# Kernel tuning notes

Hardware: AMD Instinct MI355X
Metric: run time of the kernel (lower is better)

## Reference

```python
import jax, jax.numpy as jnp
import numpy as np

B, S, P, D, L = 8, 224, 14, 512, 6
NPS = S // P            # 16 patches per side
N = NPS * NPS           # 256 tokens
G = L - 1               # 5 feedforward groups
H = D * 4
TOKEN_ATTEND_SELF_VALUE = -0.0005


def setup_inputs() -> dict:
    key = jax.random.key(0)
    k = jax.random.split(key, 8)
    s = 0.02
    f = jnp.float32
    return {
        "img": jax.random.normal(k[0], (B, 3, S, S), f),
        "W_patch": jax.random.normal(k[1], (P * P * 3, D), f) * s,
        "b_patch": jnp.zeros((D,), f),
        "pos_emb": jax.random.normal(k[2], (N, D), f) * s,
        "init_levels": jax.random.normal(k[3], (L, D), f),
        "bu_W1": jax.random.normal(k[4], (G, D, H), f) * s,
        "bu_b1": jnp.zeros((G, H), f),
        "bu_W2": jax.random.normal(k[5], (G, H, D), f) * s,
        "bu_b2": jnp.zeros((G, D), f),
        "td_W1": jax.random.normal(k[6], (G, D, H), f) * s,
        "td_b1": jnp.zeros((G, H), f),
        "td_W2": jax.random.normal(k[7], (G, H, D), f) * s,
        "td_b2": jnp.zeros((G, D), f),
        "iters": 12,
    }


def _grouped_ff(x, W1, b1, W2, b2):
    # x: [b, n, G, d]; grouped 1x1 conv == independent per-level MLP
    h = jax.nn.gelu(jnp.einsum('bnld,ldh->bnlh', x, W1) + b1, approximate=False)
    return jnp.einsum('bnlh,lhd->bnld', h, W2) + b2


def _consensus(levels):
    # levels: [b, n, L, d]; q = levels, k = l2-normalized levels, v = levels
    d = levels.shape[-1]
    norm = jnp.maximum(jnp.linalg.norm(levels, axis=-1, keepdims=True), 1e-12)
    k = levels / norm
    sim = jnp.einsum('bild,bjld->blij', levels, k) * (d ** -0.5)
    n = levels.shape[1]
    eye = jnp.eye(n, dtype=bool)[None, None]
    sim = jnp.where(eye, TOKEN_ATTEND_SELF_VALUE, sim)  # attend_self=False
    attn = jax.nn.softmax(sim, axis=-1)
    return jnp.einsum('blij,bjld->bild', attn, levels)


def _forward(img, W_patch, b_patch, pos_emb, init_levels,
             bu_W1, bu_b1, bu_W2, bu_b2, td_W1, td_b1, td_W2, td_b2, iters):
    b = img.shape[0]
    # 'b c (h p1) (w p2) -> b (h w) (p1 p2 c)'
    x = img.reshape(b, 3, NPS, P, NPS, P).transpose(0, 2, 4, 3, 5, 1).reshape(b, N, P * P * 3)
    tokens = x @ W_patch + b_patch                  # [b, n, d]
    bottom = tokens[:, :, None, :]                  # [b, n, 1, d]
    levels = jnp.broadcast_to(init_levels, (b, N, L, D)).astype(img.dtype)
    pos = pos_emb[None, :, None, :]
    contrib = jnp.array([4.0] * (L - 1) + [3.0], jnp.float32).reshape(1, 1, L, 1)

    def step(lv, _):
        lw = jnp.concatenate([bottom, lv], axis=-2)                 # [b, n, L+1, d]
        bu = _grouped_ff(lw[..., 1:-1, :], bu_W1, bu_b1, bu_W2, bu_b2)
        td = _grouped_ff(lw[..., 2:, :] + pos, td_W1, td_b1, td_W2, td_b2)
        bu = jnp.concatenate([bottom, bu], axis=-2)                 # [b, n, L, d]
        td = jnp.pad(td, ((0, 0), (0, 0), (0, 1), (0, 0)))          # [b, n, L, d]
        cons = _consensus(lv)
        new = (lv + bu + td + cons) / contrib
        return new, None

    levels, _ = jax.lax.scan(step, levels, None, length=iters)
    return levels


def reference(img, W_patch, b_patch, pos_emb, init_levels,
              bu_W1, bu_b1, bu_W2, bu_b2, td_W1, td_b1, td_W2, td_b2, iters):
    return _forward(img, W_patch, b_patch, pos_emb, init_levels,
                    bu_W1, bu_b1, bu_W2, bu_b2, td_W1, td_b1, td_W2, td_b2, iters)
```

## Files before the change

kernel.cpp:

```cpp
#include <hip/hip_runtime.h>
#include <math.h>

#define L6 6

typedef __attribute__((ext_vector_type(8))) short bf16x8;
typedef __attribute__((ext_vector_type(4))) float f32x4;

#define SH_W_GRP   2097152ull
#define SH_A_GRP   2097152ull
#define SH_A_TDOFF 10485760ull

__device__ __forceinline__ float gelu_exact(float x) {
  return 0.5f * x * (1.0f + erff(x * 0.70710678118654752f));
}

__device__ __forceinline__ unsigned short bf16_rn(float x) {
  unsigned u = __float_as_uint(x);
  unsigned r = u + 0x7FFFu + ((u >> 16) & 1u);
  return (unsigned short)(r >> 16);
}
__device__ __forceinline__ float bf16_f(unsigned short h) {
  return __uint_as_float(((unsigned)h) << 16);
}
__device__ __forceinline__ void split2(float x, unsigned short* h, unsigned short* l) {
  unsigned short hh = bf16_rn(x);
  *h = hh;
  *l = bf16_rn(x - bf16_f(hh));
}
__device__ __forceinline__ int4 pack8(const unsigned short* v) {
  return make_int4((int)((unsigned)v[0] | ((unsigned)v[1] << 16)),
                   (int)((unsigned)v[2] | ((unsigned)v[3] << 16)),
                   (int)((unsigned)v[4] | ((unsigned)v[5] << 16)),
                   (int)((unsigned)v[6] | ((unsigned)v[7] << 16)));
}

__device__ __forceinline__ void gload16(const void* g, void* l) {
  __builtin_amdgcn_global_load_lds(
      (const __attribute__((address_space(1))) void*)g,
      (__attribute__((address_space(3))) void*)l, 16, 0, 0);
}

__global__ __launch_bounds__(256) void patch_embed(
    const float* __restrict__ img, const float* __restrict__ Wp,
    const float* __restrict__ bp, float* __restrict__ tokens)
{
  __shared__ float xs[588];
  const int bn = blockIdx.x;
  const int b = bn >> 8, n = bn & 255;
  const int i = n >> 4, j = n & 15;
  for (int k = threadIdx.x; k < 588; k += 256) {
    int c = k % 3;
    int t = k / 3;
    int pc = t % 14;
    int pr = t / 14;
    xs[k] = img[(((size_t)(b * 3 + c) * 224) + (i * 14 + pr)) * 224 + (j * 14 + pc)];
  }
  __syncthreads();
  const int d0 = threadIdx.x, d1 = threadIdx.x + 256;
  float a0 = 0.f, a1 = 0.f;
  for (int k = 0; k < 588; ++k) {
    float x = xs[k];
    a0 = fmaf(x, Wp[(size_t)k * 512 + d0], a0);
    a1 = fmaf(x, Wp[(size_t)k * 512 + d1], a1);
  }
  tokens[(size_t)bn * 512 + d0] = a0 + bp[d0];
  tokens[(size_t)bn * 512 + d1] = a1 + bp[d1];
}

__global__ __launch_bounds__(256) void init_lv_kernel(
    const float* __restrict__ initl, float* __restrict__ lv)
{
  int f = blockIdx.x * 256 + threadIdx.x;
  int d4 = f & 127;
  int l = (f >> 15) % 6;
  float4 v = *(const float4*)(initl + (size_t)l * 512 + d4 * 4);
  *(float4*)(lv + (size_t)f * 4) = v;
}

__global__ __launch_bounds__(256) void norm0_k(
    const float* __restrict__ lv, float* __restrict__ invn)
{
  int bl = blockIdx.x;
  int n = threadIdx.x;
  const float* row = lv + ((size_t)bl * 256 + n) * 512;
  float ss = 0.f;
  for (int k = 0; k < 512; k += 4) {
    float4 v = *(const float4*)(row + k);
    ss = fmaf(v.x, v.x, ss);
    ss = fmaf(v.y, v.y, ss);
    ss = fmaf(v.z, v.z, ss);
    ss = fmaf(v.w, v.w, ss);
  }
  invn[(size_t)bl * 256 + n] = 1.0f / fmaxf(sqrtf(ss), 1e-12f);
}

__global__ __launch_bounds__(256) void pack_w(
    const float* __restrict__ src, short* __restrict__ dst, int KT, int NT)
{
  int sidx = blockIdx.x * 256 + threadIdx.x;
  int slot = sidx & 511;
  int blk = sidx >> 9;
  int kt = blk % KT;
  int rest = blk / KT;
  int nt = rest % NT;
  int g = rest / NT;
  int f = slot >> 6, lane = slot & 63;
  int N = NT * 128, K = KT * 32;
  int n = nt * 128 + f * 16 + (lane & 15);
  int k0 = kt * 32 + (lane >> 4) * 8;
  const float* s = src + ((size_t)g * K + k0) * N + n;
  unsigned short hi[8], lo[8];
#pragma unroll
  for (int j = 0; j < 8; ++j) split2(s[(size_t)j * N], &hi[j], &lo[j]);
  short* d = dst + (size_t)blk * 8192 + slot * 8;
  *(int4*)d = pack8(hi);
  *(int4*)(d + 4096) = pack8(lo);
}

__global__ __launch_bounds__(256) void pack_A(
    const float* __restrict__ lv, const float* __restrict__ pos,
    short* __restrict__ Abu, short* __restrict__ Atd)
{
  const int bx = blockIdx.x;
  const int lg = bx >> 8, mt = (bx >> 4) & 15, kt = bx & 15;
  const size_t blk = (size_t)bx * 8192;
#pragma unroll
  for (int ss = 0; ss < 2; ++ss) {
    int s = threadIdx.x + ss * 256;
    int f = s >> 6, l = s & 63;
    int m = mt * 128 + (f << 4) + (l & 15);
    int b = m >> 8, n = m & 255;
    int d = kt * 32 + ((l >> 4) << 3);
    const float* pbu = lv + ((size_t)(b * L6 + lg) * 256 + n) * 512 + d;
    const float* ptd = lv + ((size_t)(b * L6 + lg + 1) * 256 + n) * 512 + d;
    const float* pp = pos + (size_t)n * 512 + d;
    float4 u0 = *(const float4*)pbu;
    float4 u1 = *(const float4*)(pbu + 4);
    float xv[8] = {u0.x, u0.y, u0.z, u0.w, u1.x, u1.y, u1.z, u1.w};
    unsigned short hi[8], lo[8];
#pragma unroll
    for (int j = 0; j < 8; ++j) split2(xv[j], &hi[j], &lo[j]);
    *(int4*)(Abu + blk + s * 8) = pack8(hi);
    *(int4*)(Abu + blk + 4096 + s * 8) = pack8(lo);
    float4 v0 = *(const float4*)ptd;
    float4 v1 = *(const float4*)(ptd + 4);
    float4 p0 = *(const float4*)pp;
    float4 p1 = *(const float4*)(pp + 4);
    float yv[8] = {v0.x + p0.x, v0.y + p0.y, v0.z + p0.z, v0.w + p0.w,
                   v1.x + p1.x, v1.y + p1.y, v1.z + p1.z, v1.w + p1.w};
#pragma unroll
    for (int j = 0; j < 8; ++j) split2(yv[j], &hi[j], &lo[j]);
    *(int4*)(Atd + blk + s * 8) = pack8(hi);
    *(int4*)(Atd + blk + 4096 + s * 8) = pack8(lo);
  }
}

__global__ __launch_bounds__(256, 3) void ff1_k(
    const short* __restrict__ Wa, const short* __restrict__ Ap,
    const float* __restrict__ b1, short* __restrict__ hpk)
{
  __shared__ __align__(16) short SA[8192];
  __shared__ __align__(16) short SB[8192];
  const int per_x = gridDim.x >> 3;
  const int gid = (blockIdx.x & 7) * per_x + (blockIdx.x >> 3);
  const int tt = gid & 15;
  const int tile = gid >> 4;
  const int ht = tile & 15;
  const int z = tile >> 4;
  const int tid = threadIdx.x, lane = tid & 63, w = tid >> 6;
  const int wm = (w >> 1) * 64, wn = (w & 1) * 64;
  const short* ga = Wa + (size_t)(z * 16 + ht) * 16 * 8192;
  const short* gb = Ap + (size_t)(z * 16 + tt) * 16 * 8192;
  const int soff = w * 4096 + lane * 16;

  f32x4 acc[4][4];
#pragma unroll
  for (int i = 0; i < 4; ++i)
#pragma unroll
    for (int j = 0; j < 4; ++j) acc[i][j] = (f32x4)(0.0f);

  for (int kt = 0; kt < 16; ++kt) {
    __syncthreads();
    const char* pa = (const char*)(ga + (size_t)kt * 8192);
    const char* pb = (const char*)(gb + (size_t)kt * 8192);
#pragma unroll
    for (int c = 0; c < 4; ++c) {
      gload16(pa + soff + c * 1024, (char*)SA + w * 4096 + c * 1024);
      gload16(pb + soff + c * 1024, (char*)SB + w * 4096 + c * 1024);
    }
    __syncthreads();
    bf16x8 ah[4], al[4];
#pragma unroll
    for (int i = 0; i < 4; ++i) {
      int f = (wm >> 4) + i;
      ah[i] = *(const bf16x8*)&SA[f * 512 + lane * 8];
      al[i] = *(const bf16x8*)&SA[4096 + f * 512 + lane * 8];
    }
#pragma unroll
    for (int jp = 0; jp < 2; ++jp) {
      bf16x8 bh[2], bl[2];
#pragma unroll
      for (int j2 = 0; j2 < 2; ++j2) {
        int f = (wn >> 4) + jp * 2 + j2;
        bh[j2] = *(const bf16x8*)&SB[f * 512 + lane * 8];
        bl[j2] = *(const bf16x8*)&SB[4096 + f * 512 + lane * 8];
      }
#pragma unroll
      for (int j2 = 0; j2 < 2; ++j2)
#pragma unroll
        for (int i = 0; i < 4; ++i)
          acc[i][jp * 2 + j2] = __builtin_amdgcn_mfma_f32_16x16x32_bf16(
              ah[i], bh[j2], acc[i][jp * 2 + j2], 0, 0, 0);
#pragma unroll
      for (int j2 = 0; j2 < 2; ++j2)
#pragma unroll
        for (int i = 0; i < 4; ++i)
          acc[i][jp * 2 + j2] = __builtin_amdgcn_mfma_f32_16x16x32_bf16(
              al[i], bh[j2], acc[i][jp * 2 + j2], 0, 0, 0);
#pragma unroll
      for (int j2 = 0; j2 < 2; ++j2)
#pragma unroll
        for (int i = 0; i < 4; ++i)
          acc[i][jp * 2 + j2] = __builtin_amdgcn_mfma_f32_16x16x32_bf16(
              ah[i], bl[j2], acc[i][jp * 2 + j2], 0, 0, 0);
    }
  }

  const int q = lane >> 4, t = lane & 15;
  const float* b1g = b1 + (size_t)z * 2048;
#pragma unroll
  for (int i = 0; i < 4; ++i) {
    int Hb = ht * 128 + wm + i * 16 + q * 4;
    float4 bv = *(const float4*)(b1g + Hb);
    float bb[4] = {bv.x, bv.y, bv.z, bv.w};
    int kt2 = Hb >> 5;
    int g2 = (Hb >> 3) & 3;
    int jb = Hb & 7;
    size_t blkbase = ((size_t)(z * 16 + tt) * 64 + kt2) * 8192;
#pragma unroll
    for (int j = 0; j < 4; ++j) {
      int f2 = (wn >> 4) + j;
      size_t off = blkbase + (size_t)(f2 * 64 + g2 * 16 + t) * 8 + jb;
      unsigned short hi[4], lo[4];
#pragma unroll
      for (int r = 0; r < 4; ++r) {
        float x = gelu_exact(acc[i][j][r] + bb[r]);
        split2(x, &hi[r], &lo[r]);
      }
      *(uint2*)(hpk + off) =
          make_uint2((unsigned)hi[0] | ((unsigned)hi[1] << 16),
                     (unsigned)hi[2] | ((unsigned)hi[3] << 16));
      *(uint2*)(hpk + off + 4096) =
          make_uint2((unsigned)lo[0] | ((unsigned)lo[1] << 16),
                     (unsigned)lo[2] | ((unsigned)lo[3] << 16));
    }
  }
}

__global__ __launch_bounds__(256, 3) void attn_k(
    const float* __restrict__ lv, const short* __restrict__ Apk,
    const float* __restrict__ invn, float* __restrict__ attnb)
{
  __shared__ __align__(16) short Bhi[8192];
  __shared__ __align__(16) short Blo[8192];
  __shared__ float scL[256];
  __shared__ float red[32][4];
  const int a = blockIdx.x;
  const int s = a >> 3;
  const int b = a & 7;
  const int l = s >> 3;
  const int bl = b * 6 + l;
  const int i0 = (s & 7) * 32;
  const float* base = lv + (size_t)bl * 131072;
  const int tid = threadIdx.x, lane = tid & 63, w = tid >> 6;
  const int q = lane >> 4, c = lane & 15;

  scL[tid] = invn[(size_t)bl * 256 + tid];

  f32x4 acc[2][4];
#pragma unroll
  for (int i = 0; i < 2; ++i)
#pragma unroll
    for (int j = 0; j < 4; ++j) acc[i][j] = (f32x4)(0.0f);

  const short* src0 = Apk + ((size_t)(l * 16 + 2 * b) * 16) * 8192;
  const short* src1 = Apk + ((size_t)(l * 16 + 2 * b + 1) * 16) * 8192;

  for (int kt = 0; kt < 16; ++kt) {
    __syncthreads();
    if (l < 5) {
      const char* p0 = (const char*)(src0 + (size_t)kt * 8192);
      const char* p1 = (const char*)(src1 + (size_t)kt * 8192);
      gload16(p0 + tid * 16,         (char*)Bhi + tid * 16);
      gload16(p0 + 4096 + tid * 16,  (char*)Bhi + 4096 + tid * 16);
      gload16(p0 + 8192 + tid * 16,  (char*)Blo + tid * 16);
      gload16(p0 + 12288 + tid * 16, (char*)Blo + 4096 + tid * 16);
      gload16(p1 + tid * 16,         (char*)Bhi + 8192 + tid * 16);
      gload16(p1 + 4096 + tid * 16,  (char*)Bhi + 12288 + tid * 16);
      gload16(p1 + 8192 + tid * 16,  (char*)Blo + 8192 + tid * 16);
      gload16(p1 + 12288 + tid * 16, (char*)Blo + 12288 + tid * 16);
    } else {
      const int k0 = kt * 32;
#pragma unroll
      for (int it = 0; it < 8; ++it) {
        int f = it * 256 + tid;
        int j = f >> 3, c4 = f & 7;
        float4 v = *(const float4*)(base + (size_t)j * 512 + k0 + c4 * 4);
        unsigned short hi[4], lo[4];
        split2(v.x, &hi[0], &lo[0]);
        split2(v.y, &hi[1], &lo[1]);
        split2(v.z, &hi[2], &lo[2]);
        split2(v.w, &hi[3], &lo[3]);
        int fg = j >> 4;
        int la = (c4 >> 1) * 16 + (j & 15);
        int half = (c4 & 1) * 4;
        *(uint2*)&Bhi[fg * 512 + la * 8 + half] =
            make_uint2((unsigned)hi[0] | ((unsigned)hi[1] << 16),
                       (unsigned)hi[2] | ((unsigned)hi[3] << 16));
        *(uint2*)&Blo[fg * 512 + la * 8 + half] =
            make_uint2((unsigned)lo[0] | ((unsigned)lo[1] << 16),
                       (unsigned)lo[2] | ((unsigned)lo[3] << 16));
      }
    }
    __syncthreads();
    bf16x8 ah[2], al[2], bh[4], blv[4];
#pragma unroll
    for (int i = 0; i < 2; ++i) {
      int fg = (i0 >> 4) + i;
      ah[i] = *(const bf16x8*)&Bhi[fg * 512 + lane * 8];
      al[i] = *(const bf16x8*)&Blo[fg * 512 + lane * 8];
    }
#pragma unroll
    for (int j = 0; j < 4; ++j) {
      int fg = w * 4 + j;
      bh[j] = *(const bf16x8*)&Bhi[fg * 512 + lane * 8];
      blv[j] = *(const bf16x8*)&Blo[fg * 512 + lane * 8];
    }
#pragma unroll
    for (int j = 0; j < 4; ++j)
#pragma unroll
      for (int i = 0; i < 2; ++i)
        acc[i][j] = __builtin_amdgcn_mfma_f32_16x16x32_bf16(
            ah[i], bh[j], acc[i][j], 0, 0, 0);
#pragma unroll
    for (int j = 0; j < 4; ++j)
#pragma unroll
      for (int i = 0; i < 2; ++i)
        acc[i][j] = __builtin_amdgcn_mfma_f32_16x16x32_bf16(
            al[i], bh[j], acc[i][j], 0, 0, 0);
#pragma unroll
    for (int j = 0; j < 4; ++j)
#pragma unroll
      for (int i = 0; i < 2; ++i)
        acc[i][j] = __builtin_amdgcn_mfma_f32_16x16x32_bf16(
            ah[i], blv[j], acc[i][j], 0, 0, 0);
  }
  __syncthreads();

  const float rs = 0.04419417382415922f;
#pragma unroll
  for (int ai = 0; ai < 2; ++ai)
#pragma unroll
    for (int bj = 0; bj < 4; ++bj)
#pragma unroll
      for (int r = 0; r < 4; ++r) {
        int i = i0 + ai * 16 + q * 4 + r;
        int j = w * 64 + bj * 16 + c;
        float sv = acc[ai][bj][r] * scL[j] * rs;
        if (j == i) sv = -0.0005f;
        acc[ai][bj][r] = sv;
      }
  float mx[2][4];
#pragma unroll
  for (int ai = 0; ai < 2; ++ai)
#pragma unroll
    for (int r = 0; r < 4; ++r) {
      float m = fmaxf(fmaxf(acc[ai][0][r], acc[ai][1][r]),
                      fmaxf(acc[ai][2][r], acc[ai][3][r]));
      m = fmaxf(m, __shfl_xor(m, 1));
      m = fmaxf(m, __shfl_xor(m, 2));
      m = fmaxf(m, __shfl_xor(m, 4));
      m = fmaxf(m, __shfl_xor(m, 8));
      mx[ai][r] = m;
    }
  if (c == 0) {
#pragma unroll
    for (int ai = 0; ai < 2; ++ai)
#pragma unroll
      for (int r = 0; r < 4; ++r) red[ai * 16 + q * 4 + r][w] = mx[ai][r];
  }
  __syncthreads();
#pragma unroll
  for (int ai = 0; ai < 2; ++ai)
#pragma unroll
    for (int r = 0; r < 4; ++r) {
      int row = ai * 16 + q * 4 + r;
      mx[ai][r] = fmaxf(fmaxf(red[row][0], red[row][1]),
                        fmaxf(red[row][2], red[row][3]));
    }
  __syncthreads();
  float sm[2][4];
#pragma unroll
  for (int ai = 0; ai < 2; ++ai)
#pragma unroll
    for (int r = 0; r < 4; ++r) {
      float t = 0.f;
#pragma unroll
      for (int bj = 0; bj < 4; ++bj) {
        float e = expf(acc[ai][bj][r] - mx[ai][r]);
        acc[ai][bj][r] = e;
        t += e;
      }
      t += __shfl_xor(t, 1);
      t += __shfl_xor(t, 2);
      t += __shfl_xor(t, 4);
      t += __shfl_xor(t, 8);
      sm[ai][r] = t;
    }
  if (c == 0) {
#pragma unroll
    for (int ai = 0; ai < 2; ++ai)
#pragma unroll
      for (int r = 0; r < 4; ++r) red[ai * 16 + q * 4 + r][w] = sm[ai][r];
  }
  __syncthreads();
  float* ob = attnb + (size_t)bl * 65536;
#pragma unroll
  for (int ai = 0; ai < 2; ++ai)
#pragma unroll
    for (int r = 0; r < 4; ++r) {
      int row = ai * 16 + q * 4 + r;
      float S = red[row][0] + red[row][1] + red[row][2] + red[row][3];
      float inv = 1.0f / S;
      int i = i0 + row;
#pragma unroll
      for (int bj = 0; bj < 4; ++bj) {
        int j = w * 64 + bj * 16 + c;
        ob[(size_t)i * 256 + j] = acc[ai][bj][r] * inv;
      }
    }
}

__global__ __launch_bounds__(256) void cons_k(
    const float* __restrict__ attnb, const float* __restrict__ lv,
    float* __restrict__ accum)
{
  __shared__ __align__(16) char smemraw[25088];
  const int a = blockIdx.x;
  const int s = a >> 3;
  const int bl = (a & 7) * 6 + (s >> 4);
  const int tile = s & 15;
  int it0 = (tile >> 2) * 64;
  int dt0 = (tile & 3) * 128;
  const float* A = attnb + (size_t)bl * 65536;
  const float* Bm = lv + (size_t)bl * 131072;
  float (*Ast)[68] = (float(*)[68])smemraw;
  float (*Bs)[128] = (float(*)[128])(smemraw + 8704);
  const int tid = threadIdx.x;
  const int ty = tid >> 4, tx = tid & 15;
  float acc[4][8];
#pragma unroll
  for (int i = 0; i < 4; ++i)
#pragma unroll
    for (int j = 0; j < 8; ++j) acc[i][j] = 0.f;

  for (int k0 = 0; k0 < 256; k0 += 32) {
#pragma unroll
    for (int it = 0; it < 2; ++it) {
      int f = it * 256 + tid;
      int r = f >> 3, c4 = f & 7;
      float4 v = *(const float4*)(A + (size_t)(it0 + r) * 256 + k0 + c4 * 4);
      Ast[c4 * 4 + 0][r] = v.x;
      Ast[c4 * 4 + 1][r] = v.y;
      Ast[c4 * 4 + 2][r] = v.z;
      Ast[c4 * 4 + 3][r] = v.w;
    }
#pragma unroll
    for (int it = 0; it < 4; ++it) {
      int kr = (tid >> 5) + it * 8;
      int c4 = tid & 31;
      *(float4*)&Bs[kr][c4 * 4] =
          *(const float4*)(Bm + (size_t)(k0 + kr) * 512 + dt0 + c4 * 4);
    }
    __syncthreads();
#pragma unroll 8
    for (int k = 0; k < 32; ++k) {
      float4 av = *(const float4*)&Ast[k][ty * 4];
      float4 b0 = *(const float4*)&Bs[k][tx * 4];
      float4 b1 = *(const float4*)&Bs[k][64 + tx * 4];
      float avv[4] = {av.x, av.y, av.z, av.w};
      float bv[8] = {b0.x, b0.y, b0.z, b0.w, b1.x, b1.y, b1.z, b1.w};
#pragma unroll
      for (int i = 0; i < 4; ++i)
#pragma unroll
        for (int j = 0; j < 8; ++j)
          acc[i][j] = fmaf(avv[i], bv[j], acc[i][j]);
    }
    __syncthreads();
  }
#pragma unroll
  for (int ii = 0; ii < 4; ++ii) {
    int i = it0 + ty * 4 + ii;
    float* arow = accum + (size_t)bl * 131072 + (size_t)i * 512 + dt0;
#pragma unroll
    for (int j = 0; j < 4; ++j) arow[tx * 4 + j] += acc[ii][j];
#pragma unroll
    for (int j = 0; j < 4; ++j) arow[64 + tx * 4 + j] += acc[ii][4 + j];
  }
}

__global__ __launch_bounds__(256, 4) void mfma_ff2(
    const short* __restrict__ hpk, const short* __restrict__ Wb,
    const float* __restrict__ b2, const float* __restrict__ lv,
    const float* __restrict__ tokens, float* __restrict__ accum,
    int olvbase, int emode)
{
  const int per_x = gridDim.x >> 3;
  const int gid = (blockIdx.x & 7) * per_x + (blockIdx.x >> 3);
  const int nt2 = gid & 3;
  const int tile = gid >> 2;
  const int mt2 = tile & 31;
  const int z = tile >> 5;

  __shared__ __align__(16) short SA[4096];
  __shared__ __align__(16) short SB[8192];
  const int tid = threadIdx.x, lane = tid & 63, w = tid >> 6;
  const int wm = (w >> 1) * 32, wn = (w & 1) * 64;
  const short* gaBase = hpk + (size_t)(z * 16 + (mt2 >> 1)) * 64 * 8192
                        + (size_t)(mt2 & 1) * 2048;
  const short* gb = Wb + (size_t)(z * 4 + nt2) * 64 * 8192;

  f32x4 acc[2][4];
#pragma unroll
  for (int i = 0; i < 2; ++i)
#pragma unroll
    for (int j = 0; j < 4; ++j) acc[i][j] = (f32x4)(0.0f);

  for (int kt = 0; kt < 64; ++kt) {
    __syncthreads();
    const char* pa = (const char*)(gaBase + (size_t)kt * 8192);
    const char* pb = (const char*)(gb + (size_t)kt * 8192);
    gload16(pa + w * 1024 + lane * 16, (char*)SA + w * 1024);
    gload16(pa + 8192 + w * 1024 + lane * 16, (char*)SA + 4096 + w * 1024);
#pragma unroll
    for (int c = 0; c < 4; ++c)
      gload16(pb + w * 4096 + c * 1024 + lane * 16,
              (char*)SB + w * 4096 + c * 1024);
    __syncthreads();
    bf16x8 ah[2], al[2];
#pragma unroll
    for (int i = 0; i < 2; ++i) {
      int f = (wm >> 4) + i;
      ah[i] = *(const bf16x8*)&SA[f * 512 + lane * 8];
      al[i] = *(const bf16x8*)&SA[2048 + f * 512 + lane * 8];
    }
#pragma unroll
    for (int jp = 0; jp < 2; ++jp) {
      bf16x8 bh[2], bl[2];
#pragma unroll
      for (int j2 = 0; j2 < 2; ++j2) {
        int f = (wn >> 4) + jp * 2 + j2;
        bh[j2] = *(const bf16x8*)&SB[f * 512 + lane * 8];
        bl[j2] = *(const bf16x8*)&SB[4096 + f * 512 + lane * 8];
      }
#pragma unroll
      for (int j2 = 0; j2 < 2; ++j2)
#pragma unroll
        for (int i = 0; i < 2; ++i)
          acc[i][jp * 2 + j2] = __builtin_amdgcn_mfma_f32_16x16x32_bf16(
              ah[i], bh[j2], acc[i][jp * 2 + j2], 0, 0, 0);
#pragma unroll
      for (int j2 = 0; j2 < 2; ++j2)
#pragma unroll
        for (int i = 0; i < 2; ++i)
          acc[i][jp * 2 + j2] = __builtin_amdgcn_mfma_f32_16x16x32_bf16(
              al[i], bh[j2], acc[i][jp * 2 + j2], 0, 0, 0);
#pragma unroll
      for (int j2 = 0; j2 < 2; ++j2)
#pragma unroll
        for (int i = 0; i < 2; ++i)
          acc[i][jp * 2 + j2] = __builtin_amdgcn_mfma_f32_16x16x32_bf16(
              ah[i], bl[j2], acc[i][jp * 2 + j2], 0, 0, 0);
    }
  }

  const int q = lane >> 4, t = lane & 15;
  const float* b2g = b2 + (size_t)z * 512;
  const int level = olvbase + z;
#pragma unroll
  for (int i = 0; i < 2; ++i) {
#pragma unroll
    for (int r = 0; r < 4; ++r) {
      int m = mt2 * 64 + wm + i * 16 + q * 4 + r;
      int b = m >> 8, n = m & 255;
      size_t rowoff = ((size_t)(b * L6 + level) * 256 + n) * 512;
      float* arow = accum + rowoff;
      const float* lrow = lv + rowoff;
      const float* trow = tokens + (size_t)m * 512;
#pragma unroll
      for (int j = 0; j < 4; ++j) {
        int col = nt2 * 128 + wn + j * 16 + t;
        float v = acc[i][j][r] + b2g[col];
        if (emode == 0)                       arow[col] = lrow[col] + v;
        else if (level == 0)                  arow[col] = lrow[col] + trow[col] + v;
        else                                  arow[col] += v;
      }
    }
  }
}

__global__ __launch_bounds__(256) void combine3(
    const float* __restrict__ accum, const float* __restrict__ pos,
    float* __restrict__ lv_out, short* __restrict__ Abu,
    short* __restrict__ Atd, float* __restrict__ invn,
    float* __restrict__ dout, int last)
{
  int t = blockIdx.x * 256 + threadIdx.x;
  int d8 = t & 63;
  int n = (t >> 6) & 255;
  int v = t >> 14;
  int l = v % 6, b = v / 6;
  int bn = (b << 8) | n;
  size_t idx = ((size_t)v * 256 + n) * 512 + d8 * 8;
  float4 a0 = *(const float4*)(accum + idx);
  float4 a1 = *(const float4*)(accum + idx + 4);
  float sc = (l == 5) ? (1.0f / 3.0f) : 0.25f;
  float r[8];
  r[0] = a0.x * sc; r[1] = a0.y * sc; r[2] = a0.z * sc; r[3] = a0.w * sc;
  r[4] = a1.x * sc; r[5] = a1.y * sc; r[6] = a1.z * sc; r[7] = a1.w * sc;
  *(float4*)(lv_out + idx) = make_float4(r[0], r[1], r[2], r[3]);
  *(float4*)(lv_out + idx + 4) = make_float4(r[4], r[5], r[6], r[7]);
  if (last) {
    float* dp = dout + ((size_t)bn * 6 + l) * 512 + d8 * 8;
    *(float4*)dp = make_float4(r[0], r[1], r[2], r[3]);
    *(float4*)(dp + 4) = make_float4(r[4], r[5], r[6], r[7]);
  }
  {
    float s8 = 0.f;
#pragma unroll
    for (int j = 0; j < 8; ++j) s8 = fmaf(r[j], r[j], s8);
#pragma unroll
    for (int o = 1; o < 64; o <<= 1) s8 += __shfl_xor(s8, o);
    if (d8 == 0) invn[(size_t)v * 256 + n] = 1.0f / fmaxf(sqrtf(s8), 1e-12f);
  }
  int m = bn;
  int mt = m >> 7;
  int kt = d8 >> 2;
  int s = (((m & 127) >> 4) << 6) | (((d8 & 3) << 4) | (m & 15));
  unsigned short hi[8], lo[8];
  if (l < 5) {
    size_t blk = ((size_t)(l * 16 + mt) * 16 + kt) * 8192;
#pragma unroll
    for (int j = 0; j < 8; ++j) split2(r[j], &hi[j], &lo[j]);
    *(int4*)(Abu + blk + s * 8) = pack8(hi);
    *(int4*)(Abu + blk + 4096 + s * 8) = pack8(lo);
  }
  if (l >= 1) {
    const float* pp = pos + (size_t)n * 512 + d8 * 8;
    float4 p0 = *(const float4*)pp;
    float4 p1 = *(const float4*)(pp + 4);
    float y[8] = {r[0] + p0.x, r[1] + p0.y, r[2] + p0.z, r[3] + p0.w,
                  r[4] + p1.x, r[5] + p1.y, r[6] + p1.z, r[7] + p1.w};
    size_t blk = ((size_t)((l - 1) * 16 + mt) * 16 + kt) * 8192;
#pragma unroll
    for (int j = 0; j < 8; ++j) split2(y[j], &hi[j], &lo[j]);
    *(int4*)(Atd + blk + s * 8) = pack8(hi);
    *(int4*)(Atd + blk + 4096 + s * 8) = pack8(lo);
  }
}

extern "C" void kernel_launch(void* const* d_in, const int* in_sizes, int n_in,
                              void* d_out, int out_size, void* d_ws, size_t ws_size,
                              hipStream_t stream)
{
  const float* img   = (const float*)d_in[0];
  const float* Wp    = (const float*)d_in[1];
  const float* bp    = (const float*)d_in[2];
  const float* pos   = (const float*)d_in[3];
  const float* initl = (const float*)d_in[4];
  const float* buW1  = (const float*)d_in[5];
  const float* bub1  = (const float*)d_in[6];
  const float* buW2  = (const float*)d_in[7];
  const float* bub2  = (const float*)d_in[8];
  const float* tdW1  = (const float*)d_in[9];
  const float* tdb1  = (const float*)d_in[10];
  const float* tdW2  = (const float*)d_in[11];
  const float* tdb2  = (const float*)d_in[12];

  float* ws = (float*)d_ws;
  const size_t LV = (size_t)8 * 6 * 256 * 512;
  float* lv     = ws;
  float* tokens = lv + LV;
  float* accum  = tokens + 1048576ull;
  short* W1all  = (short*)(accum + LV);
  short* W2all  = W1all + 20971520ull;
  short* Apk    = W2all + 20971520ull;
  short* hall   = Apk + 20971520ull;
  float* invn   = (float*)(hall + 41943040ull);

  float* attnb = (float*)(hall + 20971520ull);
  float* dout  = (float*)d_out;

  pack_w<<<2560, 256, 0, stream>>>(buW1, W1all, 16, 16);
  pack_w<<<2560, 256, 0, stream>>>(tdW1, W1all + 5 * SH_W_GRP, 16, 16);
  pack_w<<<2560, 256, 0, stream>>>(buW2, W2all, 64, 4);
  pack_w<<<2560, 256, 0, stream>>>(tdW2, W2all + 5 * SH_W_GRP, 64, 4);

  patch_embed<<<2048, 256, 0, stream>>>(img, Wp, bp, tokens);
  init_lv_kernel<<<6144, 256, 0, stream>>>(initl, lv);
  norm0_k<<<48, 256, 0, stream>>>(lv, invn);
  pack_A<<<1280, 256, 0, stream>>>(lv, pos, Apk, Apk + SH_A_TDOFF);

  for (int it = 0; it < 12; ++it) {
    ff1_k<<<1280, 256, 0, stream>>>(W1all, Apk, bub1, hall);
    mfma_ff2<<<640, 256, 0, stream>>>(hall, W2all, bub2, lv, tokens, accum, 1, 0);
    ff1_k<<<1280, 256, 0, stream>>>(W1all + 5 * SH_W_GRP, Apk + SH_A_TDOFF,
                                    tdb1, hall);
    mfma_ff2<<<640, 256, 0, stream>>>(hall, W2all + 5 * SH_W_GRP, tdb2, lv,
                                      tokens, accum, 0, 1);
    attn_k<<<384, 256, 0, stream>>>(lv, Apk, invn, attnb);
    cons_k<<<768, 256, 0, stream>>>(attnb, lv, accum);
    combine3<<<3072, 256, 0, stream>>>(accum, pos, lv, Apk, Apk + SH_A_TDOFF,
                                       invn, dout, it == 11 ? 1 : 0);
  }
}
```

Before: 4.731 ms.

## Load MFMA fragments directly from global memory, dropping LDS staging in FF GEMMs

Both grouped-FF GEMM kernels (ff1 and ff2) previously staged A and B tiles through shared memory with two barriers per k-step. They now read each wave's pre-packed bf16 fragments straight from global memory into registers and feed the MFMAs. This removes LDS traffic and the block-wide syncs. In exchange, operands that several waves share are now fetched from global memory/L2 once per wave instead of once per block, and global load latency is exposed without explicit double buffering.

```diff
diff --git a/kernel.cpp b/kernel.cpp
--- a/kernel.cpp
+++ b/kernel.cpp
@@ -159,8 +159,6 @@
     const short* __restrict__ Wa, const short* __restrict__ Ap,
     const float* __restrict__ b1, short* __restrict__ hpk)
 {
-  __shared__ __align__(16) short SA[8192];
-  __shared__ __align__(16) short SB[8192];
   const int per_x = gridDim.x >> 3;
   const int gid = (blockIdx.x & 7) * per_x + (blockIdx.x >> 3);
   const int tt = gid & 15;
@@ -169,9 +167,8 @@
   const int z = tile >> 4;
   const int tid = threadIdx.x, lane = tid & 63, w = tid >> 6;
   const int wm = (w >> 1) * 64, wn = (w & 1) * 64;
-  const short* ga = Wa + (size_t)(z * 16 + ht) * 16 * 8192;
-  const short* gb = Ap + (size_t)(z * 16 + tt) * 16 * 8192;
-  const int soff = w * 4096 + lane * 16;
+  const short* ga = Wa + (size_t)(z * 16 + ht) * 16 * 8192 + (wm << 5) + lane * 8;
+  const short* gb = Ap + (size_t)(z * 16 + tt) * 16 * 8192 + (wn << 5) + lane * 8;
 
   f32x4 acc[4][4];
 #pragma unroll
@@ -180,50 +177,37 @@
     for (int j = 0; j < 4; ++j) acc[i][j] = (f32x4)(0.0f);
 
   for (int kt = 0; kt < 16; ++kt) {
-    __syncthreads();
-    const char* pa = (const char*)(ga + (size_t)kt * 8192);
-    const char* pb = (const char*)(gb + (size_t)kt * 8192);
-#pragma unroll
-    for (int c = 0; c < 4; ++c) {
-      gload16(pa + soff + c * 1024, (char*)SA + w * 4096 + c * 1024);
-      gload16(pb + soff + c * 1024, (char*)SB + w * 4096 + c * 1024);
-    }
-    __syncthreads();
-    bf16x8 ah[4], al[4];
+    const short* pa = ga + (size_t)kt * 8192;
+    const short* pb = gb + (size_t)kt * 8192;
+    bf16x8 ah[4], al[4], bh[4], bl[4];
 #pragma unroll
     for (int i = 0; i < 4; ++i) {
-      int f = (wm >> 4) + i;
-      ah[i] = *(const bf16x8*)&SA[f * 512 + lane * 8];
-      al[i] = *(const bf16x8*)&SA[4096 + f * 512 + lane * 8];
-    }
-#pragma unroll
-    for (int jp = 0; jp < 2; ++jp) {
-      bf16x8 bh[2], bl[2];
-#pragma unroll
-      for (int j2 = 0; j2 < 2; ++j2) {
-        int f = (wn >> 4) + jp * 2 + j2;
-        bh[j2] = *(const bf16x8*)&SB[f * 512 + lane * 8];
-        bl[j2] = *(const bf16x8*)&SB[4096 + f * 512 + lane * 8];
-      }
-#pragma unroll
-      for (int j2 = 0; j2 < 2; ++j2)
-#pragma unroll
-        for (int i = 0; i < 4; ++i)
-          acc[i][jp * 2 + j2] = __builtin_amdgcn_mfma_f32_16x16x32_bf16(
-              ah[i], bh[j2], acc[i][jp * 2 + j2], 0, 0, 0);
-#pragma unroll
-      for (int j2 = 0; j2 < 2; ++j2)
-#pragma unroll
-        for (int i = 0; i < 4; ++i)
-          acc[i][jp * 2 + j2] = __builtin_amdgcn_mfma_f32_16x16x32_bf16(
-              al[i], bh[j2], acc[i][jp * 2 + j2], 0, 0, 0);
-#pragma unroll
-      for (int j2 = 0; j2 < 2; ++j2)
-#pragma unroll
-        for (int i = 0; i < 4; ++i)
-          acc[i][jp * 2 + j2] = __builtin_amdgcn_mfma_f32_16x16x32_bf16(
-              ah[i], bl[j2], acc[i][jp * 2 + j2], 0, 0, 0);
-    }
+      ah[i] = *(const bf16x8*)(pa + i * 512);
+      al[i] = *(const bf16x8*)(pa + 4096 + i * 512);
+    }
+#pragma unroll
+    for (int j = 0; j < 4; ++j) {
+      bh[j] = *(const bf16x8*)(pb + j * 512);
+      bl[j] = *(const bf16x8*)(pb + 4096 + j * 512);
+    }
+#pragma unroll
+    for (int j = 0; j < 4; ++j)
+#pragma unroll
+      for (int i = 0; i < 4; ++i)
+        acc[i][j] = __builtin_amdgcn_mfma_f32_16x16x32_bf16(
+            ah[i], bh[j], acc[i][j], 0, 0, 0);
+#pragma unroll
+    for (int j = 0; j < 4; ++j)
+#pragma unroll
+      for (int i = 0; i < 4; ++i)
+        acc[i][j] = __builtin_amdgcn_mfma_f32_16x16x32_bf16(
+            al[i], bh[j], acc[i][j], 0, 0, 0);
+#pragma unroll
+    for (int j = 0; j < 4; ++j)
+#pragma unroll
+      for (int i = 0; i < 4; ++i)
+        acc[i][j] = __builtin_amdgcn_mfma_f32_16x16x32_bf16(
+            ah[i], bl[j], acc[i][j], 0, 0, 0);
   }
 
   const int q = lane >> 4, t = lane & 15;
@@ -522,13 +506,12 @@
   const int mt2 = tile & 31;
   const int z = tile >> 5;
 
-  __shared__ __align__(16) short SA[4096];
-  __shared__ __align__(16) short SB[8192];
   const int tid = threadIdx.x, lane = tid & 63, w = tid >> 6;
   const int wm = (w >> 1) * 32, wn = (w & 1) * 64;
-  const short* gaBase = hpk + (size_t)(z * 16 + (mt2 >> 1)) * 64 * 8192
-                        + (size_t)(mt2 & 1) * 2048;
-  const short* gb = Wb + (size_t)(z * 4 + nt2) * 64 * 8192;
+  const short* ga = hpk + (size_t)(z * 16 + (mt2 >> 1)) * 64 * 8192
+                    + (size_t)(mt2 & 1) * 2048 + (wm << 5) + lane * 8;
+  const short* gb = Wb + (size_t)(z * 4 + nt2) * 64 * 8192
+                    + (wn << 5) + lane * 8;
 
   f32x4 acc[2][4];
 #pragma unroll
@@ -537,51 +520,37 @@
     for (int j = 0; j < 4; ++j) acc[i][j] = (f32x4)(0.0f);
 
   for (int kt = 0; kt < 64; ++kt) {
-    __syncthreads();
-    const char* pa = (const char*)(gaBase + (size_t)kt * 8192);
-    const char* pb = (const char*)(gb + (size_t)kt * 8192);
-    gload16(pa + w * 1024 + lane * 16, (char*)SA + w * 1024);
-    gload16(pa + 8192 + w * 1024 + lane * 16, (char*)SA + 4096 + w * 1024);
-#pragma unroll
-    for (int c = 0; c < 4; ++c)
-      gload16(pb + w * 4096 + c * 1024 + lane * 16,
-              (char*)SB + w * 4096 + c * 1024);
-    __syncthreads();
-    bf16x8 ah[2], al[2];
+    const short* pa = ga + (size_t)kt * 8192;
+    const short* pb = gb + (size_t)kt * 8192;
+    bf16x8 ah[2], al[2], bh[4], bl[4];
 #pragma unroll
     for (int i = 0; i < 2; ++i) {
-      int f = (wm >> 4) + i;
-      ah[i] = *(const bf16x8*)&SA[f * 512 + lane * 8];
-      al[i] = *(const bf16x8*)&SA[2048 + f * 512 + lane * 8];
-    }
-#pragma unroll
-    for (int jp = 0; jp < 2; ++jp) {
-      bf16x8 bh[2], bl[2];
-#pragma unroll
-      for (int j2 = 0; j2 < 2; ++j2) {
-        int f = (wn >> 4) + jp * 2 + j2;
-        bh[j2] = *(const bf16x8*)&SB[f * 512 + lane * 8];
-        bl[j2] = *(const bf16x8*)&SB[4096 + f * 512 + lane * 8];
-      }
-#pragma unroll
-      for (int j2 = 0; j2 < 2; ++j2)
-#pragma unroll
-        for (int i = 0; i < 2; ++i)
-          acc[i][jp * 2 + j2] = __builtin_amdgcn_mfma_f32_16x16x32_bf16(
-              ah[i], bh[j2], acc[i][jp * 2 + j2], 0, 0, 0);
-#pragma unroll
-      for (int j2 = 0; j2 < 2; ++j2)
-#pragma unroll
-        for (int i = 0; i < 2; ++i)
-          acc[i][jp * 2 + j2] = __builtin_amdgcn_mfma_f32_16x16x32_bf16(
-              al[i], bh[j2], acc[i][jp * 2 + j2], 0, 0, 0);
-#pragma unroll
-      for (int j2 = 0; j2 < 2; ++j2)
-#pragma unroll
-        for (int i = 0; i < 2; ++i)
-          acc[i][jp * 2 + j2] = __builtin_amdgcn_mfma_f32_16x16x32_bf16(
-              ah[i], bl[j2], acc[i][jp * 2 + j2], 0, 0, 0);
-    }
+      ah[i] = *(const bf16x8*)(pa + i * 512);
+      al[i] = *(const bf16x8*)(pa + 4096 + i * 512);
+    }
+#pragma unroll
+    for (int j = 0; j < 4; ++j) {
+      bh[j] = *(const bf16x8*)(pb + j * 512);
+      bl[j] = *(const bf16x8*)(pb + 4096 + j * 512);
+    }
+#pragma unroll
+    for (int j = 0; j < 4; ++j)
+#pragma unroll
+      for (int i = 0; i < 2; ++i)
+        acc[i][j] = __builtin_amdgcn_mfma_f32_16x16x32_bf16(
+            ah[i], bh[j], acc[i][j], 0, 0, 0);
+#pragma unroll
+    for (int j = 0; j < 4; ++j)
+#pragma unroll
+      for (int i = 0; i < 2; ++i)
+        acc[i][j] = __builtin_amdgcn_mfma_f32_16x16x32_bf16(
+            al[i], bh[j], acc[i][j], 0, 0, 0);
+#pragma unroll
+    for (int j = 0; j < 4; ++j)
+#pragma unroll
+      for (int i = 0; i < 2; ++i)
+        acc[i][j] = __builtin_amdgcn_mfma_f32_16x16x32_bf16(
+            ah[i], bl[j], acc[i][j], 0, 0, 0);
   }
 
   const int q = lane >> 4, t = lane & 15;
```

Result: slower. 5.324 ms (+12.5%).
